# Kernel tuning notes

Hardware: AMD Instinct MI355X
Metric: run time of the kernel (lower is better)

The kernel has to match this reference:

```python
import jax, jax.numpy as jnp
import numpy as np

N_NODES = 50000
N_EDGES = 1600000
IN_DIM = 6
H = 64


def _sage_conv(x, src, dst, W_l, b_l, W_r, num_nodes):
    """PyG SAGEConv (aggr='mean'): out = lin_l(mean_{j in N(i)} x_j) + lin_r(x_i).
    lin_l has bias, lin_r has no bias (PyG default)."""
    # mean-aggregate neighbor features at destination nodes
    agg = jax.ops.segment_sum(x[src], dst, num_segments=num_nodes)          # [N, d]
    cnt = jax.ops.segment_sum(jnp.ones((src.shape[0],), x.dtype), dst,
                              num_segments=num_nodes)                        # [N]
    mean = agg / jnp.maximum(cnt, 1.0)[:, None]
    return mean @ W_l + b_l + x @ W_r


def setup_inputs() -> dict:
    key = jax.random.key(0)
    ks = jax.random.split(key, 8)
    x = jax.random.normal(ks[0], (N_NODES, IN_DIM), dtype=jnp.float32)
    edge_index = jax.random.randint(ks[1], (2, N_EDGES), 0, N_NODES, dtype=jnp.int64)
    # Kaiming-ish scaled params
    def lin(k, fan_in, fan_out):
        return jax.random.normal(k, (fan_in, fan_out), dtype=jnp.float32) / np.sqrt(fan_in)
    return {
        "x": x,
        "edge_index": edge_index,
        "W1_l": lin(ks[2], IN_DIM, H),
        "b1_l": jnp.zeros((H,), jnp.float32),
        "W1_r": lin(ks[3], IN_DIM, H),
        "W2_l": lin(ks[4], H, H),
        "b2_l": jnp.zeros((H,), jnp.float32),
        "W2_r": lin(ks[5], H, H),
    }


def reference(x, edge_index, W1_l, b1_l, W1_r, W2_l, b2_l, W2_r):
    src, dst = edge_index[0], edge_index[1]
    n = x.shape[0]
    z = jax.nn.relu(_sage_conv(x, src, dst, W1_l, b1_l, W1_r, n))  # [N, H]
    z = _sage_conv(z, src, dst, W2_l, b2_l, W2_r, n)               # [N, H]
    return z
```

## Files before the change

### kernel.cpp

```cpp
#include <hip/hip_runtime.h>

#define N_NODES 50000
#define N_EDGES 1600000
#define IN_DIM 6
#define H 64

#define NBUCKET 196
#define NBLK 196
#define EPB 8192
#define BCAP 9216

#define L2PAD 72

__device__ __forceinline__ float bf2f(unsigned short u) {
    return __uint_as_float(((unsigned int)u) << 16);
}
__device__ __forceinline__ unsigned short f2bf(float f) {
    unsigned int u = __float_as_uint(f);
    u += 0x7fffu + ((u >> 16) & 1u);
    return (unsigned short)(u >> 16);
}

__global__ __launch_bounds__(256) void scatter_bucketed(
        const int* __restrict__ ei,
        int* __restrict__ gcur,
        unsigned int* __restrict__ ebin,
        const float* __restrict__ W2l,
        const float* __restrict__ W2r,
        unsigned short* __restrict__ Wlt,
        unsigned short* __restrict__ Wrt,
        unsigned short* __restrict__ z) {
    int t = threadIdx.x;
    if (blockIdx.x == NBLK) {
        for (int i = t; i < H * H; i += 256) {
            int k = i >> 6, f = i & 63;
            Wlt[f * H + k] = f2bf(W2l[i]);
            Wrt[f * H + k] = f2bf(W2r[i]);
        }
        if (t < H) z[(size_t)N_NODES * H + t] = 0;
        return;
    }
    __shared__ unsigned int sedge[EPB];
    __shared__ int hist[NBUCKET];
    __shared__ int cur[NBUCKET];
    for (int i = t; i < NBUCKET; i += 256) hist[i] = 0;
    __syncthreads();
    int e0 = blockIdx.x * EPB;
    int cnt = min(EPB, N_EDGES - e0);
    const int4* s4 = (const int4*)(ei + e0);
    const int4* d4 = (const int4*)(ei + N_EDGES + e0);
    for (int k = t; k * 4 < cnt; k += 256) {
        int4 sv = s4[k];
        int4 dv = d4[k];
        sedge[k * 4 + 0] = ((unsigned)sv.x << 16) | (unsigned)dv.x;
        sedge[k * 4 + 1] = ((unsigned)sv.y << 16) | (unsigned)dv.y;
        sedge[k * 4 + 2] = ((unsigned)sv.z << 16) | (unsigned)dv.z;
        sedge[k * 4 + 3] = ((unsigned)sv.w << 16) | (unsigned)dv.w;
        atomicAdd(&hist[dv.x >> 8], 1);
        atomicAdd(&hist[dv.y >> 8], 1);
        atomicAdd(&hist[dv.z >> 8], 1);
        atomicAdd(&hist[dv.w >> 8], 1);
    }
    __syncthreads();
    for (int i = t; i < NBUCKET; i += 256)
        cur[i] = atomicAdd(&gcur[i], hist[i]);
    __syncthreads();
    for (int k = t; k * 4 < cnt; k += 256) {
#pragma unroll
        for (int j = 0; j < 4; j++) {
            unsigned int p = sedge[k * 4 + j];
            int b = (int)(p & 0xffffu) >> 8;
            int pos = atomicAdd(&cur[b], 1);
            if (pos < BCAP) ebin[(size_t)b * BCAP + pos] = p;
        }
    }
}

__global__ __launch_bounds__(512) void bucket_layer1(
        const unsigned int* __restrict__ ebin,
        const int* __restrict__ gcur,
        const float* __restrict__ x,
        const float* __restrict__ W1l,
        const float* __restrict__ b1,
        const float* __restrict__ W1r,
        int2* __restrict__ rowpair,
        unsigned short* __restrict__ esrc,
        unsigned short* __restrict__ z) {
    __shared__ int raw[BCAP];
    __shared__ unsigned short ssrc[BCAP];
    __shared__ int sdeg[256];
    __shared__ int sstart[256];
    __shared__ int scur[256];
    __shared__ int wsum[4];
    __shared__ float sW1l[IN_DIM * H];
    __shared__ float sW1r[IN_DIM * H];
    float* smx   = (float*)raw;
    float* spart = (float*)raw + 4096;

    int t = threadIdx.x;
    int lane = t & 63, w = t >> 6;
    int b = blockIdx.x;
    int base = b << 8;
    int nn = min(256, N_NODES - base);
    int ebase = b * BCAP;
    int cnt = min(gcur[b], BCAP);

    if (t < 256) sdeg[t] = 0;
    for (int i = t; i < IN_DIM * H; i += 512) { sW1l[i] = W1l[i]; sW1r[i] = W1r[i]; }
    for (int i = t; i < cnt; i += 512) raw[i] = (int)ebin[ebase + i];
    __syncthreads();
    for (int i = t; i < cnt; i += 512) atomicAdd(&sdeg[raw[i] & 0xff], 1);
    __syncthreads();
    int v = 0, s = 0;
    if (t < 256) {
        v = sdeg[t]; s = v;
#pragma unroll
        for (int off = 1; off < 64; off <<= 1) {
            int u = __shfl_up(s, off);
            if (lane >= off) s += u;
        }
        if (lane == 63) wsum[w] = s;
    }
    __syncthreads();
    if (t < 256) {
        int woff = 0;
        for (int k = 0; k < w; k++) woff += wsum[k];
        int excl = s - v + woff;
        sstart[t] = excl;
        scur[t] = excl;
        if (t < nn) rowpair[base + t] = make_int2(ebase + excl, ebase + excl + v);
    }
    __syncthreads();
    for (int i = t; i < cnt; i += 512) {
        int p = raw[i];
        int pos = atomicAdd(&scur[p & 0xff], 1);
        ssrc[pos] = (unsigned short)((unsigned)p >> 16);
    }
    __syncthreads();
    for (int i = t; i < cnt; i += 512)
        esrc[ebase + i] = ssrc[i];
    for (int i = t; i < nn * IN_DIM; i += 512) {
        int node = i / 6, k = i - node * 6;
        smx[node * 16 + 6 + k] = x[(size_t)base * IN_DIM + i];
    }

    int node = t & 255, half = t >> 8;
    float a0 = 0.f, a1 = 0.f, a2 = 0.f, a3 = 0.f, a4 = 0.f, a5 = 0.f;
    int deg = 0, st = 0;
    if (node < nn) { deg = sdeg[node]; st = sstart[node]; }
    for (int i = st + half; i < st + deg; i += 2) {
        int src = ssrc[i];
        const float2* xs = (const float2*)(x + (size_t)src * IN_DIM);
        float2 p0 = xs[0], p1 = xs[1], p2 = xs[2];
        a0 += p0.x; a1 += p0.y; a2 += p1.x;
        a3 += p1.y; a4 += p2.x; a5 += p2.y;
    }
    if (half == 1 && node < nn) {
        spart[node * 6 + 0] = a0; spart[node * 6 + 1] = a1;
        spart[node * 6 + 2] = a2; spart[node * 6 + 3] = a3;
        spart[node * 6 + 4] = a4; spart[node * 6 + 5] = a5;
    }
    __syncthreads();
    if (half == 0 && node < nn) {
        float inv = 1.0f / fmaxf((float)deg, 1.0f);
        smx[node * 16 + 0] = (a0 + spart[node * 6 + 0]) * inv;
        smx[node * 16 + 1] = (a1 + spart[node * 6 + 1]) * inv;
        smx[node * 16 + 2] = (a2 + spart[node * 6 + 2]) * inv;
        smx[node * 16 + 3] = (a3 + spart[node * 6 + 3]) * inv;
        smx[node * 16 + 4] = (a4 + spart[node * 6 + 4]) * inv;
        smx[node * 16 + 5] = (a5 + spart[node * 6 + 5]) * inv;
    }
    __syncthreads();

    int feat = t & 63, ng = t >> 6;
    float wl[IN_DIM], wr[IN_DIM];
#pragma unroll
    for (int k = 0; k < IN_DIM; k++) { wl[k] = sW1l[k * H + feat]; wr[k] = sW1r[k * H + feat]; }
    float bias = b1[feat];
    for (int nb = ng; nb < nn; nb += 8) {
        const float4* row = (const float4*)&smx[nb * 16];
        float4 r0 = row[0], r1 = row[1], r2 = row[2];
        float acc = bias;
        acc += r0.x * wl[0] + r0.y * wl[1] + r0.z * wl[2]
             + r0.w * wl[3] + r1.x * wl[4] + r1.y * wl[5];
        acc += r1.z * wr[0] + r1.w * wr[1] + r2.x * wr[2]
             + r2.y * wr[3] + r2.z * wr[4] + r2.w * wr[5];
        z[(size_t)(base + nb) * H + feat] = f2bf(fmaxf(acc, 0.0f));
    }
}

__global__ __launch_bounds__(256) void layer2_mfma(
        const unsigned short* __restrict__ zin,
        const int2* __restrict__ rowpair,
        const unsigned short* __restrict__ esrc,
        const unsigned short* __restrict__ Wlt,
        const float* __restrict__ b2,
        const unsigned short* __restrict__ Wrt,
        float* __restrict__ out) {
    typedef short bf16x8 __attribute__((ext_vector_type(8)));
    typedef float f32x4 __attribute__((ext_vector_type(4)));
    __shared__ __attribute__((aligned(16))) unsigned short smean[16 * L2PAD];
    __shared__ __attribute__((aligned(16))) unsigned short szl[16 * L2PAD];
    __shared__ __attribute__((aligned(16))) unsigned short sWl[64 * L2PAD];
    __shared__ __attribute__((aligned(16))) unsigned short sWr[64 * L2PAD];

    int t = threadIdx.x;
    int w = t >> 6, lane = t & 63;
    int g = lane >> 4, lg = lane & 15;
    int n0 = blockIdx.x * 16;

    {
        const ushort4* wl4 = (const ushort4*)Wlt;
        const ushort4* wr4 = (const ushort4*)Wrt;
        for (int qi = t; qi < H * H / 4; qi += 256) {
            int f = qi >> 4, kq = qi & 15;
            *(ushort4*)&sWl[f * L2PAD + kq * 4] = wl4[qi];
            *(ushort4*)&sWr[f * L2PAD + kq * 4] = wr4[qi];
        }
    }

    for (int q = 0; q < 4; q++) {
        int ln = w * 4 + q;
        int n = n0 + ln;
        int2 rp = rowpair[n];
        int r0 = rp.x, r1 = rp.y;
        float4 acc = make_float4(0.f, 0.f, 0.f, 0.f);
        for (int base = r0; base < r1; base += 64) {
            int ii = base + lane;
            int idx = (ii < r1) ? (int)esrc[ii] : N_NODES;
            int rem = r1 - base;
#pragma unroll 1
            for (int c = 0; c < 64; c += 16) {
                if (c >= rem) break;
#pragma unroll
                for (int tt = 0; tt < 4; tt++) {
                    int j = c + tt * 4 + g;
                    int s = __shfl(idx, j);
                    const ushort4* zr = (const ushort4*)(zin + (size_t)s * H);
                    ushort4 vv = zr[lg];
                    acc.x += bf2f(vv.x); acc.y += bf2f(vv.y);
                    acc.z += bf2f(vv.z); acc.w += bf2f(vv.w);
                }
            }
        }
#pragma unroll
        for (int off = 16; off < 64; off <<= 1) {
            acc.x += __shfl_xor(acc.x, off);
            acc.y += __shfl_xor(acc.y, off);
            acc.z += __shfl_xor(acc.z, off);
            acc.w += __shfl_xor(acc.w, off);
        }
        float inv = 1.0f / fmaxf((float)(r1 - r0), 1.0f);
        if (g == 0) {
            ushort4 mb;
            mb.x = f2bf(acc.x * inv); mb.y = f2bf(acc.y * inv);
            mb.z = f2bf(acc.z * inv); mb.w = f2bf(acc.w * inv);
            *(ushort4*)&smean[ln * L2PAD + lg * 4] = mb;
        }
        szl[ln * L2PAD + lane] = zin[(size_t)n * H + lane];
    }
    __syncthreads();

    f32x4 acc = {0.f, 0.f, 0.f, 0.f};
#pragma unroll
    for (int ks = 0; ks < 2; ks++) {
        int ko = ks * 32 + g * 8;
        bf16x8 aM = *(const bf16x8*)&smean[lg * L2PAD + ko];
        bf16x8 aZ = *(const bf16x8*)&szl[lg * L2PAD + ko];
        bf16x8 bL = *(const bf16x8*)&sWl[(w * 16 + lg) * L2PAD + ko];
        bf16x8 bR = *(const bf16x8*)&sWr[(w * 16 + lg) * L2PAD + ko];
        acc = __builtin_amdgcn_mfma_f32_16x16x32_bf16(aM, bL, acc, 0, 0, 0);
        acc = __builtin_amdgcn_mfma_f32_16x16x32_bf16(aZ, bR, acc, 0, 0, 0);
    }
    float bias = b2[w * 16 + lg];
#pragma unroll
    for (int r = 0; r < 4; r++) {
        int node = n0 + g * 4 + r;
        out[(size_t)node * H + w * 16 + lg] = acc[r] + bias;
    }
}

extern "C" void kernel_launch(void* const* d_in, const int* in_sizes, int n_in,
                              void* d_out, int out_size, void* d_ws, size_t ws_size,
                              hipStream_t stream) {
    const float* x   = (const float*)d_in[0];
    const int*   ei  = (const int*)d_in[1];
    const float* W1l = (const float*)d_in[2];
    const float* b1  = (const float*)d_in[3];
    const float* W1r = (const float*)d_in[4];
    const float* W2l = (const float*)d_in[5];
    const float* b2  = (const float*)d_in[6];
    const float* W2r = (const float*)d_in[7];
    float* out = (float*)d_out;

    int* gcur = (int*)d_ws;
    int2* rowpair = (int2*)(gcur + 208);
    unsigned int*   ebin = (unsigned int*)(rowpair + N_NODES);
    unsigned short* esrc = (unsigned short*)(ebin + (size_t)NBUCKET * BCAP);
    unsigned short* z    = esrc + (size_t)NBUCKET * BCAP;
    unsigned short* Wlt  = z + (size_t)(N_NODES + 1) * H;
    unsigned short* Wrt  = Wlt + H * H;

    hipMemsetAsync(gcur, 0, NBUCKET * sizeof(int), stream);

    scatter_bucketed<<<NBLK + 1, 256, 0, stream>>>(ei, gcur, ebin,
                                                   W2l, W2r, Wlt, Wrt, z);
    bucket_layer1<<<NBUCKET, 512, 0, stream>>>(ebin, gcur, x, W1l, b1, W1r,
                                               rowpair, esrc, z);
    layer2_mfma<<<N_NODES / 16, 256, 0, stream>>>(z, rowpair, esrc,
                                                  Wlt, b2, Wrt, out);
}
```

Measured before the change: 152.2 us.

## Use finer node buckets, smaller edge chunks, and 32-node layer-2 blocks

Halves the bucket size to 128 destination nodes (391 buckets) and splits edges into 500 chunks of 3200, so the scatter and layer-1 kernels launch more, smaller blocks on the 256-CU GPU. Layer-1 now splits each node's edges over four thread groups and reduces the partial sums through shared memory. Layer-2 handles 32 nodes per 512-thread block, with bounds checks for the ragged tail, so the staged bf16 weights are reused across more nodes. The price is more global atomics on the bucket counters and a tighter per-bucket capacity (BCAP), which assumes the degree distribution stays near uniform.

```diff
diff --git a/kernel.cpp b/kernel.cpp
--- a/kernel.cpp
+++ b/kernel.cpp
@@ -5,10 +5,12 @@
 #define IN_DIM 6
 #define H 64
 
-#define NBUCKET 196
-#define NBLK 196
-#define EPB 8192
-#define BCAP 9216
+#define BSHIFT 7
+#define BNODES 128
+#define NBUCKET 391
+#define BCAP 4736
+#define NCHUNK 500
+#define EPB 3200
 
 #define L2PAD 72
 
@@ -31,7 +33,7 @@
         unsigned short* __restrict__ Wrt,
         unsigned short* __restrict__ z) {
     int t = threadIdx.x;
-    if (blockIdx.x == NBLK) {
+    if (blockIdx.x == NCHUNK) {
         for (int i = t; i < H * H; i += 256) {
             int k = i >> 6, f = i & 63;
             Wlt[f * H + k] = f2bf(W2l[i]);
@@ -46,30 +48,29 @@
     for (int i = t; i < NBUCKET; i += 256) hist[i] = 0;
     __syncthreads();
     int e0 = blockIdx.x * EPB;
-    int cnt = min(EPB, N_EDGES - e0);
     const int4* s4 = (const int4*)(ei + e0);
     const int4* d4 = (const int4*)(ei + N_EDGES + e0);
-    for (int k = t; k * 4 < cnt; k += 256) {
+    for (int k = t; k * 4 < EPB; k += 256) {
         int4 sv = s4[k];
         int4 dv = d4[k];
         sedge[k * 4 + 0] = ((unsigned)sv.x << 16) | (unsigned)dv.x;
         sedge[k * 4 + 1] = ((unsigned)sv.y << 16) | (unsigned)dv.y;
         sedge[k * 4 + 2] = ((unsigned)sv.z << 16) | (unsigned)dv.z;
         sedge[k * 4 + 3] = ((unsigned)sv.w << 16) | (unsigned)dv.w;
-        atomicAdd(&hist[dv.x >> 8], 1);
-        atomicAdd(&hist[dv.y >> 8], 1);
-        atomicAdd(&hist[dv.z >> 8], 1);
-        atomicAdd(&hist[dv.w >> 8], 1);
+        atomicAdd(&hist[dv.x >> BSHIFT], 1);
+        atomicAdd(&hist[dv.y >> BSHIFT], 1);
+        atomicAdd(&hist[dv.z >> BSHIFT], 1);
+        atomicAdd(&hist[dv.w >> BSHIFT], 1);
     }
     __syncthreads();
     for (int i = t; i < NBUCKET; i += 256)
         cur[i] = atomicAdd(&gcur[i], hist[i]);
     __syncthreads();
-    for (int k = t; k * 4 < cnt; k += 256) {
+    for (int k = t; k * 4 < EPB; k += 256) {
 #pragma unroll
         for (int j = 0; j < 4; j++) {
             unsigned int p = sedge[k * 4 + j];
-            int b = (int)(p & 0xffffu) >> 8;
+            int b = (int)(p & 0xffffu) >> BSHIFT;
             int pos = atomicAdd(&cur[b], 1);
             if (pos < BCAP) ebin[(size_t)b * BCAP + pos] = p;
         }
@@ -86,33 +87,33 @@
         int2* __restrict__ rowpair,
         unsigned short* __restrict__ esrc,
         unsigned short* __restrict__ z) {
-    __shared__ int raw[BCAP];
+    __shared__ __attribute__((aligned(16))) int raw[BCAP];
     __shared__ unsigned short ssrc[BCAP];
-    __shared__ int sdeg[256];
-    __shared__ int sstart[256];
-    __shared__ int scur[256];
-    __shared__ int wsum[4];
+    __shared__ int sdeg[BNODES];
+    __shared__ int sstart[BNODES];
+    __shared__ int scur[BNODES];
+    __shared__ int wsum[2];
     __shared__ float sW1l[IN_DIM * H];
     __shared__ float sW1r[IN_DIM * H];
     float* smx   = (float*)raw;
-    float* spart = (float*)raw + 4096;
+    float* spart = (float*)raw + 2048;
 
     int t = threadIdx.x;
     int lane = t & 63, w = t >> 6;
     int b = blockIdx.x;
-    int base = b << 8;
-    int nn = min(256, N_NODES - base);
+    int base = b << BSHIFT;
+    int nn = min(BNODES, N_NODES - base);
     int ebase = b * BCAP;
     int cnt = min(gcur[b], BCAP);
 
-    if (t < 256) sdeg[t] = 0;
-    for (int i = t; i < IN_DIM * H; i += 512) { sW1l[i] = W1l[i]; sW1r[i] = W1r[i]; }
+    if (t < BNODES) sdeg[t] = 0;
+    if (t < IN_DIM * H) { sW1l[t] = W1l[t]; sW1r[t] = W1r[t]; }
     for (int i = t; i < cnt; i += 512) raw[i] = (int)ebin[ebase + i];
     __syncthreads();
-    for (int i = t; i < cnt; i += 512) atomicAdd(&sdeg[raw[i] & 0xff], 1);
+    for (int i = t; i < cnt; i += 512) atomicAdd(&sdeg[raw[i] & (BNODES - 1)], 1);
     __syncthreads();
     int v = 0, s = 0;
-    if (t < 256) {
+    if (t < BNODES) {
         v = sdeg[t]; s = v;
 #pragma unroll
         for (int off = 1; off < 64; off <<= 1) {
@@ -122,9 +123,8 @@
         if (lane == 63) wsum[w] = s;
     }
     __syncthreads();
-    if (t < 256) {
-        int woff = 0;
-        for (int k = 0; k < w; k++) woff += wsum[k];
+    if (t < BNODES) {
+        int woff = (w == 1) ? wsum[0] : 0;
         int excl = s - v + woff;
         sstart[t] = excl;
         scur[t] = excl;
@@ -133,7 +133,7 @@
     __syncthreads();
     for (int i = t; i < cnt; i += 512) {
         int p = raw[i];
-        int pos = atomicAdd(&scur[p & 0xff], 1);
+        int pos = atomicAdd(&scur[p & (BNODES - 1)], 1);
         ssrc[pos] = (unsigned short)((unsigned)p >> 16);
     }
     __syncthreads();
@@ -144,31 +144,33 @@
         smx[node * 16 + 6 + k] = x[(size_t)base * IN_DIM + i];
     }
 
-    int node = t & 255, half = t >> 8;
+    int node = t & (BNODES - 1), q = t >> BSHIFT;
     float a0 = 0.f, a1 = 0.f, a2 = 0.f, a3 = 0.f, a4 = 0.f, a5 = 0.f;
     int deg = 0, st = 0;
     if (node < nn) { deg = sdeg[node]; st = sstart[node]; }
-    for (int i = st + half; i < st + deg; i += 2) {
+    for (int i = st + q; i < st + deg; i += 4) {
         int src = ssrc[i];
         const float2* xs = (const float2*)(x + (size_t)src * IN_DIM);
         float2 p0 = xs[0], p1 = xs[1], p2 = xs[2];
         a0 += p0.x; a1 += p0.y; a2 += p1.x;
         a3 += p1.y; a4 += p2.x; a5 += p2.y;
     }
-    if (half == 1 && node < nn) {
-        spart[node * 6 + 0] = a0; spart[node * 6 + 1] = a1;
-        spart[node * 6 + 2] = a2; spart[node * 6 + 3] = a3;
-        spart[node * 6 + 4] = a4; spart[node * 6 + 5] = a5;
-    }
-    __syncthreads();
-    if (half == 0 && node < nn) {
+    if (q > 0 && node < nn) {
+        float* sp = &spart[(q - 1) * (BNODES * 6) + node * 6];
+        sp[0] = a0; sp[1] = a1; sp[2] = a2; sp[3] = a3; sp[4] = a4; sp[5] = a5;
+    }
+    __syncthreads();
+    if (q == 0 && node < nn) {
         float inv = 1.0f / fmaxf((float)deg, 1.0f);
-        smx[node * 16 + 0] = (a0 + spart[node * 6 + 0]) * inv;
-        smx[node * 16 + 1] = (a1 + spart[node * 6 + 1]) * inv;
-        smx[node * 16 + 2] = (a2 + spart[node * 6 + 2]) * inv;
-        smx[node * 16 + 3] = (a3 + spart[node * 6 + 3]) * inv;
-        smx[node * 16 + 4] = (a4 + spart[node * 6 + 4]) * inv;
-        smx[node * 16 + 5] = (a5 + spart[node * 6 + 5]) * inv;
+        const float* p1p = &spart[0 * (BNODES * 6) + node * 6];
+        const float* p2p = &spart[1 * (BNODES * 6) + node * 6];
+        const float* p3p = &spart[2 * (BNODES * 6) + node * 6];
+        smx[node * 16 + 0] = (a0 + p1p[0] + p2p[0] + p3p[0]) * inv;
+        smx[node * 16 + 1] = (a1 + p1p[1] + p2p[1] + p3p[1]) * inv;
+        smx[node * 16 + 2] = (a2 + p1p[2] + p2p[2] + p3p[2]) * inv;
+        smx[node * 16 + 3] = (a3 + p1p[3] + p2p[3] + p3p[3]) * inv;
+        smx[node * 16 + 4] = (a4 + p1p[4] + p2p[4] + p3p[4]) * inv;
+        smx[node * 16 + 5] = (a5 + p1p[5] + p2p[5] + p3p[5]) * inv;
     }
     __syncthreads();
 
@@ -189,7 +191,7 @@
     }
 }
 
-__global__ __launch_bounds__(256) void layer2_mfma(
+__global__ __launch_bounds__(512) void layer2_mfma(
         const unsigned short* __restrict__ zin,
         const int2* __restrict__ rowpair,
         const unsigned short* __restrict__ esrc,
@@ -199,20 +201,20 @@
         float* __restrict__ out) {
     typedef short bf16x8 __attribute__((ext_vector_type(8)));
     typedef float f32x4 __attribute__((ext_vector_type(4)));
-    __shared__ __attribute__((aligned(16))) unsigned short smean[16 * L2PAD];
-    __shared__ __attribute__((aligned(16))) unsigned short szl[16 * L2PAD];
+    __shared__ __attribute__((aligned(16))) unsigned short smean[32 * L2PAD];
+    __shared__ __attribute__((aligned(16))) unsigned short szl[32 * L2PAD];
     __shared__ __attribute__((aligned(16))) unsigned short sWl[64 * L2PAD];
     __shared__ __attribute__((aligned(16))) unsigned short sWr[64 * L2PAD];
 
     int t = threadIdx.x;
     int w = t >> 6, lane = t & 63;
     int g = lane >> 4, lg = lane & 15;
-    int n0 = blockIdx.x * 16;
+    int n0 = blockIdx.x * 32;
 
     {
         const ushort4* wl4 = (const ushort4*)Wlt;
         const ushort4* wr4 = (const ushort4*)Wrt;
-        for (int qi = t; qi < H * H / 4; qi += 256) {
+        for (int qi = t; qi < H * H / 4; qi += 512) {
             int f = qi >> 4, kq = qi & 15;
             *(ushort4*)&sWl[f * L2PAD + kq * 4] = wl4[qi];
             *(ushort4*)&sWr[f * L2PAD + kq * 4] = wr4[qi];
@@ -222,8 +224,9 @@
     for (int q = 0; q < 4; q++) {
         int ln = w * 4 + q;
         int n = n0 + ln;
-        int2 rp = rowpair[n];
-        int r0 = rp.x, r1 = rp.y;
+        bool valid = (n < N_NODES);
+        int r0 = 0, r1 = 0;
+        if (valid) { int2 rp = rowpair[n]; r0 = rp.x; r1 = rp.y; }
         float4 acc = make_float4(0.f, 0.f, 0.f, 0.f);
         for (int base = r0; base < r1; base += 64) {
             int ii = base + lane;
@@ -257,26 +260,29 @@
             mb.z = f2bf(acc.z * inv); mb.w = f2bf(acc.w * inv);
             *(ushort4*)&smean[ln * L2PAD + lg * 4] = mb;
         }
-        szl[ln * L2PAD + lane] = zin[(size_t)n * H + lane];
-    }
-    __syncthreads();
-
+        int nz = valid ? n : N_NODES;
+        szl[ln * L2PAD + lane] = zin[(size_t)nz * H + lane];
+    }
+    __syncthreads();
+
+    int nb = w >> 2, fb = w & 3;
     f32x4 acc = {0.f, 0.f, 0.f, 0.f};
 #pragma unroll
     for (int ks = 0; ks < 2; ks++) {
         int ko = ks * 32 + g * 8;
-        bf16x8 aM = *(const bf16x8*)&smean[lg * L2PAD + ko];
-        bf16x8 aZ = *(const bf16x8*)&szl[lg * L2PAD + ko];
-        bf16x8 bL = *(const bf16x8*)&sWl[(w * 16 + lg) * L2PAD + ko];
-        bf16x8 bR = *(const bf16x8*)&sWr[(w * 16 + lg) * L2PAD + ko];
+        bf16x8 aM = *(const bf16x8*)&smean[(nb * 16 + lg) * L2PAD + ko];
+        bf16x8 aZ = *(const bf16x8*)&szl[(nb * 16 + lg) * L2PAD + ko];
+        bf16x8 bL = *(const bf16x8*)&sWl[(fb * 16 + lg) * L2PAD + ko];
+        bf16x8 bR = *(const bf16x8*)&sWr[(fb * 16 + lg) * L2PAD + ko];
         acc = __builtin_amdgcn_mfma_f32_16x16x32_bf16(aM, bL, acc, 0, 0, 0);
         acc = __builtin_amdgcn_mfma_f32_16x16x32_bf16(aZ, bR, acc, 0, 0, 0);
     }
-    float bias = b2[w * 16 + lg];
+    float bias = b2[fb * 16 + lg];
 #pragma unroll
     for (int r = 0; r < 4; r++) {
-        int node = n0 + g * 4 + r;
-        out[(size_t)node * H + w * 16 + lg] = acc[r] + bias;
+        int node = n0 + nb * 16 + g * 4 + r;
+        if (node < N_NODES)
+            out[(size_t)node * H + fb * 16 + lg] = acc[r] + bias;
     }
 }
 
@@ -294,7 +300,7 @@
     float* out = (float*)d_out;
 
     int* gcur = (int*)d_ws;
-    int2* rowpair = (int2*)(gcur + 208);
+    int2* rowpair = (int2*)(gcur + 400);
     unsigned int*   ebin = (unsigned int*)(rowpair + N_NODES);
     unsigned short* esrc = (unsigned short*)(ebin + (size_t)NBUCKET * BCAP);
     unsigned short* z    = esrc + (size_t)NBUCKET * BCAP;
@@ -303,10 +309,10 @@
 
     hipMemsetAsync(gcur, 0, NBUCKET * sizeof(int), stream);
 
-    scatter_bucketed<<<NBLK + 1, 256, 0, stream>>>(ei, gcur, ebin,
-                                                   W2l, W2r, Wlt, Wrt, z);
+    scatter_bucketed<<<NCHUNK + 1, 256, 0, stream>>>(ei, gcur, ebin,
+                                                     W2l, W2r, Wlt, Wrt, z);
     bucket_layer1<<<NBUCKET, 512, 0, stream>>>(ebin, gcur, x, W1l, b1, W1r,
                                                rowpair, esrc, z);
-    layer2_mfma<<<N_NODES / 16, 256, 0, stream>>>(z, rowpair, esrc,
-                                                  Wlt, b2, Wrt, out);
-}
+    layer2_mfma<<<(N_NODES + 31) / 32, 512, 0, stream>>>(z, rowpair, esrc,
+                                                         Wlt, b2, Wrt, out);
+}
```

After: 158.4 us. +4.1%, slower.
